# Kernel optimization log

Hardware: AMD Instinct MI355X
Metric: run time of the kernel (lower is better)

The kernel has to match this reference:

```python
import jax, jax.numpy as jnp
import numpy as np
from jax.scipy.special import gammaln

B, T, U = 65536, 64, 8


def gamma_filter(tau, n, T):
    # tau, n: (1, U) already mulFac-scaled. Matches generate_simple_filter_multichan.
    t = jnp.arange(T, dtype=jnp.float32)[:, None]            # (T, 1)
    f = t ** n * jnp.exp(-t / tau)                           # (T, U); f[0]=0 since n>0
    f = f / (tau ** (n + 1.0)) / jnp.exp(gammaln(n + 1.0))
    return f                                                 # (T, U)


def causal_conv(x, K):
    # x: (B, T), K: (T, U). y[b,t,u] = sum_{j<=t} x[b,t-j] * K[j,u]
    # == tf.nn.conv2d with reversed kernel and causal left-pad (T-1, 0).
    T = x.shape[1]
    idx = jnp.arange(T)[:, None] - jnp.arange(T)[None, :]    # (T, T) = t - t'
    Kmat = jnp.where(idx[:, :, None] >= 0, K[jnp.clip(idx, 0, T - 1)], 0.0)  # (T, T, U)
    return jnp.einsum('bs,tsu->btu', x, Kmat)                # (B, T, U)


def setup_inputs() -> dict:
    key = jax.random.key(0)
    ks = jax.random.split(key, 12)
    uni = lambda k, lo, hi: jax.random.uniform(k, (1, U), minval=lo, maxval=hi, dtype=jnp.float32)
    return {
        'inputs': jax.random.uniform(ks[0], (B, T, 1), dtype=jnp.float32),  # light intensity >= 0
        'alpha': uni(ks[1], 0.001, 0.1),
        'beta':  uni(ks[2], 0.001, 0.1),
        'gamma': uni(ks[3], 0.01, 0.1),
        'zeta':  uni(ks[4], 0.0, 0.1),      # computed but unused by call()
        'tauY':  uni(ks[5], 0.001, 0.02),   # y-path is dead code (unused by outputs)
        'nY':    uni(ks[6], 1e-5, 0.1),
        'tauZ':  uni(ks[7], 0.3, 1.0),
        'nZ':    jnp.full((1, U), 0.01, jnp.float32),  # frozen constant in the layer
        'tauC':  uni(ks[8], 0.01, 0.5),
        'nC':    jnp.full((1, U), 0.01, jnp.float32),  # frozen constant in the layer
    }


def reference(inputs, alpha, beta, gamma, zeta, tauY, nY, tauZ, nZ, tauC, nC):
    Bv, Tv, P = inputs.shape  # P == 1 (pixels folded into batch)
    a = alpha * 100.0         # alpha_mulFac
    b = beta * 10.0           # beta_mulFac
    g = gamma * 10.0          # gamma_mulFac
    tau_z = tauZ * 100.0
    n_z = nZ * 10.0
    tau_c = tauC * 100.0
    n_c = nC * 10.0

    Kc = gamma_filter(tau_c, n_c, Tv)                      # (T, U)
    Kz = g[0][None, :] * Kc + (1.0 - g[0][None, :]) * gamma_filter(tau_z, n_z, Tv)

    x = inputs[:, :, 0]                                    # (B, T)
    z = causal_conv(x, Kz)                                 # (B, T, U)

    # slice_tensor: per-unit gather at flat time index (T - argmax_t Kz)
    z_shift = jnp.argmax(Kz, axis=0)                       # (U,), >=1 since Kz[0]=0
    t_idx = jnp.clip(Tv - z_shift, 0, Tv - 1)
    z_sel = z[:, t_idx, jnp.arange(U)]                     # (B, U)

    # outputs = alpha * x / (1 + beta * z), broadcast to (B, T, 1, 1, U)
    out = (a[0][None, None, None, None, :] * inputs[:, :, :, None, None]
           / (1.0 + b[0][None, None, None, None, :] * z_sel[:, None, None, None, :]))
    return out
```

## Files before the change

kernel.cpp:

```cpp
#include <hip/hip_runtime.h>
#include <math.h>

#define TSZ 64
#define USZ 8
#define NB  32
#define XS  68


__global__ void setup_kernel(const float* __restrict__ alpha,
                             const float* __restrict__ beta,
                             const float* __restrict__ gamma_,
                             const float* __restrict__ tauZ,
                             const float* __restrict__ nZ,
                             const float* __restrict__ tauC,
                             const float* __restrict__ nC,
                             float* __restrict__ ws) {
    __shared__ float kz[USZ][TSZ];
    __shared__ int ti_s[USZ];
    const int t = threadIdx.x;
    const float tf = (float)t;
    for (int u = 0; u < USZ; ++u) {
        float g     = gamma_[u] * 10.0f;
        float tau_c = tauC[u] * 100.0f;
        float n_c   = nC[u]   * 10.0f;
        float tau_z = tauZ[u] * 100.0f;
        float n_z   = nZ[u]   * 10.0f;
        float kc  = powf(tf, n_c) * expf(-tf / tau_c) / powf(tau_c, n_c + 1.0f) / tgammaf(n_c + 1.0f);
        float kzg = powf(tf, n_z) * expf(-tf / tau_z) / powf(tau_z, n_z + 1.0f) / tgammaf(n_z + 1.0f);
        kz[u][t] = g * kc + (1.0f - g) * kzg;
    }
    __syncthreads();
    if (t < USZ) {
        const int u = t;
        float best = kz[u][0];
        int bi = 0;
        for (int s = 1; s < TSZ; ++s) {
            float v = kz[u][s];
            if (v > best) { best = v; bi = s; }
        }
        int ti = TSZ - bi;
        if (ti > TSZ - 1) ti = TSZ - 1;
        if (ti < 0) ti = 0;
        ti_s[u] = ti;
        ws[512 + u] = alpha[u] * 100.0f;
        ws[520 + u] = beta[u]  * 10.0f;
    }
    __syncthreads();
    for (int u = 0; u < USZ; ++u) {
        int ti = ti_s[u];
        ws[u * TSZ + t] = (t <= ti) ? kz[u][ti - t] : 0.0f;
    }
}

__global__ __launch_bounds__(256) void main_kernel(const float* __restrict__ x,
                                                   const float* __restrict__ ws,
                                                   float* __restrict__ out) {
    __shared__ __attribute__((aligned(16))) float xs[NB * XS];
    __shared__ __attribute__((aligned(16))) float wl[USZ * XS];
    __shared__ __attribute__((aligned(16))) float fs[NB * USZ];

    const int tid = threadIdx.x;
    const int blk = blockIdx.x;

    if (tid < 128) {
        float4 v = ((const float4*)ws)[tid];
        int u  = tid >> 4;
        int s0 = (tid & 15) << 2;
        *((float4*)&wl[u * XS + s0]) = v;
    }
    const float4* x4 = (const float4*)(x + (size_t)blk * NB * TSZ);
    #pragma unroll
    for (int k = 0; k < 2; ++k) {
        int j = tid + k * 256;
        float4 v = x4[j];
        int bl = j >> 4;
        int s0 = (j & 15) << 2;
        *((float4*)&xs[bl * XS + s0]) = v;
    }
    __syncthreads();

    {
        const int bl = tid >> 3;
        const int u  = tid & 7;
        const float4* xr = (const float4*)&xs[bl * XS];
        const float4* wr = (const float4*)&wl[u * XS];
        float acc = 0.0f;
        #pragma unroll
        for (int j = 0; j < 16; ++j) {
            float4 a = xr[j];
            float4 b = wr[j];
            acc += a.x * b.x + a.y * b.y + a.z * b.z + a.w * b.w;
        }
        float av = ws[512 + u];
        float bv = ws[520 + u];
        fs[bl * USZ + u] = av / (1.0f + bv * acc);
    }
    __syncthreads();

    float4* o4 = (float4*)(out + (size_t)blk * NB * TSZ * USZ);
    #pragma unroll
    for (int k = 0; k < 16; ++k) {
        int j = tid + k * 256;
        int bl   = j >> 7;
        int r    = j & 127;
        int t    = r >> 1;
        int half = r & 1;
        float xv = xs[bl * XS + t];
        float4 f = *((const float4*)&fs[bl * USZ + half * 4]);
        float4 o;
        o.x = xv * f.x; o.y = xv * f.y; o.z = xv * f.z; o.w = xv * f.w;
        o4[j] = o;
    }
}

extern "C" void kernel_launch(void* const* d_in, const int* in_sizes, int n_in,
                              void* d_out, int out_size, void* d_ws, size_t ws_size,
                              hipStream_t stream) {
    const float* inputs = (const float*)d_in[0];
    const float* alpha  = (const float*)d_in[1];
    const float* beta   = (const float*)d_in[2];
    const float* gamma_ = (const float*)d_in[3];
    const float* tauZ   = (const float*)d_in[7];
    const float* nZ     = (const float*)d_in[8];
    const float* tauC   = (const float*)d_in[9];
    const float* nC     = (const float*)d_in[10];
    float* out = (float*)d_out;
    float* ws  = (float*)d_ws;

    setup_kernel<<<1, 64, 0, stream>>>(alpha, beta, gamma_, tauZ, nZ, tauC, nC, ws);

    const int B = in_sizes[0] / TSZ;
    main_kernel<<<B / NB, 256, 0, stream>>>(inputs, ws, out);
}
```

Measured before the change: 180.1 us.

## Parallelize setup kernel, halve batch tile, use nontemporal output stores

The setup kernel now runs 1024 threads so that every (filter, unit, time) element of the gamma filters is computed in parallel instead of looping over units serially. The main kernel tile shrinks from 32 to 16 batch rows per block, which doubles the grid, and the reduction step leaves half the threads idle. Output writes use nontemporal vector stores so the large write-only output does not pollute the cache. These changes target the serial setup latency and write bandwidth, at the cost of more blocks, each doing less work.

```diff
diff --git a/kernel.cpp b/kernel.cpp
--- a/kernel.cpp
+++ b/kernel.cpp
@@ -3,11 +3,13 @@
 
 #define TSZ 64
 #define USZ 8
-#define NB  32
+#define NB  16
 #define XS  68
 
+typedef float nfloat4 __attribute__((ext_vector_type(4)));
 
-__global__ void setup_kernel(const float* __restrict__ alpha,
+
+__global__ __launch_bounds__(1024) void setup_kernel(const float* __restrict__ alpha,
                              const float* __restrict__ beta,
                              const float* __restrict__ gamma_,
                              const float* __restrict__ tauZ,
@@ -15,23 +17,33 @@
                              const float* __restrict__ tauC,
                              const float* __restrict__ nC,
                              float* __restrict__ ws) {
+    __shared__ float kbuf[2][USZ][TSZ];
     __shared__ float kz[USZ][TSZ];
     __shared__ int ti_s[USZ];
-    const int t = threadIdx.x;
-    const float tf = (float)t;
-    for (int u = 0; u < USZ; ++u) {
-        float g     = gamma_[u] * 10.0f;
-        float tau_c = tauC[u] * 100.0f;
-        float n_c   = nC[u]   * 10.0f;
-        float tau_z = tauZ[u] * 100.0f;
-        float n_z   = nZ[u]   * 10.0f;
-        float kc  = powf(tf, n_c) * expf(-tf / tau_c) / powf(tau_c, n_c + 1.0f) / tgammaf(n_c + 1.0f);
-        float kzg = powf(tf, n_z) * expf(-tf / tau_z) / powf(tau_z, n_z + 1.0f) / tgammaf(n_z + 1.0f);
-        kz[u][t] = g * kc + (1.0f - g) * kzg;
+
+    const int tid = threadIdx.x;
+    {
+        const int fid = tid >> 9;
+        const int rem = tid & 511;
+        const int u   = rem >> 6;
+        const int t   = rem & 63;
+        const float tf = (float)t;
+        float tau, n;
+        if (fid == 0) { tau = tauC[u] * 100.0f; n = nC[u] * 10.0f; }
+        else          { tau = tauZ[u] * 100.0f; n = nZ[u] * 10.0f; }
+        float f = powf(tf, n) * expf(-tf / tau) / powf(tau, n + 1.0f) / tgammaf(n + 1.0f);
+        kbuf[fid][u][t] = f;
     }
     __syncthreads();
-    if (t < USZ) {
-        const int u = t;
+    if (tid < 512) {
+        const int u = tid >> 6;
+        const int t = tid & 63;
+        float g = gamma_[u] * 10.0f;
+        kz[u][t] = g * kbuf[0][u][t] + (1.0f - g) * kbuf[1][u][t];
+    }
+    __syncthreads();
+    if (tid < USZ) {
+        const int u = tid;
         float best = kz[u][0];
         int bi = 0;
         for (int s = 1; s < TSZ; ++s) {
@@ -46,7 +58,9 @@
         ws[520 + u] = beta[u]  * 10.0f;
     }
     __syncthreads();
-    for (int u = 0; u < USZ; ++u) {
+    if (tid < 512) {
+        const int u = tid >> 6;
+        const int t = tid & 63;
         int ti = ti_s[u];
         ws[u * TSZ + t] = (t <= ti) ? kz[u][ti - t] : 0.0f;
     }
@@ -68,18 +82,16 @@
         int s0 = (tid & 15) << 2;
         *((float4*)&wl[u * XS + s0]) = v;
     }
-    const float4* x4 = (const float4*)(x + (size_t)blk * NB * TSZ);
-    #pragma unroll
-    for (int k = 0; k < 2; ++k) {
-        int j = tid + k * 256;
-        float4 v = x4[j];
-        int bl = j >> 4;
-        int s0 = (j & 15) << 2;
+    {
+        const float4* x4 = (const float4*)(x + (size_t)blk * NB * TSZ);
+        float4 v = x4[tid];
+        int bl = tid >> 4;
+        int s0 = (tid & 15) << 2;
         *((float4*)&xs[bl * XS + s0]) = v;
     }
     __syncthreads();
 
-    {
+    if (tid < NB * USZ) {
         const int bl = tid >> 3;
         const int u  = tid & 7;
         const float4* xr = (const float4*)&xs[bl * XS];
@@ -97,9 +109,9 @@
     }
     __syncthreads();
 
-    float4* o4 = (float4*)(out + (size_t)blk * NB * TSZ * USZ);
+    nfloat4* o4 = (nfloat4*)(out + (size_t)blk * NB * TSZ * USZ);
     #pragma unroll
-    for (int k = 0; k < 16; ++k) {
+    for (int k = 0; k < 8; ++k) {
         int j = tid + k * 256;
         int bl   = j >> 7;
         int r    = j & 127;
@@ -107,9 +119,9 @@
         int half = r & 1;
         float xv = xs[bl * XS + t];
         float4 f = *((const float4*)&fs[bl * USZ + half * 4]);
-        float4 o;
+        nfloat4 o;
         o.x = xv * f.x; o.y = xv * f.y; o.z = xv * f.z; o.w = xv * f.w;
-        o4[j] = o;
+        __builtin_nontemporal_store(o, &o4[j]);
     }
 }
 
@@ -127,7 +139,7 @@
     float* out = (float*)d_out;
     float* ws  = (float*)d_ws;
 
-    setup_kernel<<<1, 64, 0, stream>>>(alpha, beta, gamma_, tauZ, nZ, tauC, nC, ws);
+    setup_kernel<<<1, 1024, 0, stream>>>(alpha, beta, gamma_, tauZ, nZ, tauC, nC, ws);
 
     const int B = in_sizes[0] / TSZ;
     main_kernel<<<B / NB, 256, 0, stream>>>(inputs, ws, out);
```

New measurement: 173.3 us. -3.7%, faster.
